# Performance work log

Hardware: AMD Instinct MI355X
Metric: run time of the kernel (lower is better)

## Reference

```python
import jax, jax.numpy as jnp
import numpy as np

HIDDEN = 2560
N_HEADS = 32
HEAD_DIM = HIDDEN // N_HEADS  # 80
ROT_DIM = int(0.4 * HEAD_DIM)  # 32, partial_rotary_factor = 0.4
MAX_POS = 2048
ROPE_THETA = 10000.0
LN_EPS = 1e-5


def _make_rope_tables(max_pos, rot_dim, theta):
    inv_freq = 1.0 / (theta ** (np.arange(0, rot_dim, 2, dtype=np.float32) / rot_dim))
    t = np.arange(max_pos, dtype=np.float32)
    freqs = np.outer(t, inv_freq)            # [max_pos, rot_dim/2]
    emb = np.concatenate([freqs, freqs], -1)  # [max_pos, rot_dim]
    return jnp.asarray(np.sin(emb)), jnp.asarray(np.cos(emb))


def setup_inputs() -> dict:
    key = jax.random.key(0)
    ks = jax.random.split(key, 16)
    B, S = 2, 2048
    std = 0.02
    sin, cos = _make_rope_tables(MAX_POS, ROT_DIM, ROPE_THETA)
    return {
        "hidden_states": jax.random.normal(ks[0], (B, S, HIDDEN), jnp.float32),
        "attention_mask": jnp.ones((B, S), jnp.int32),
        "position_ids": jnp.broadcast_to(jnp.arange(S, dtype=jnp.int32), (B, S)),
        "sin": sin, "cos": cos,
        "Wq": std * jax.random.normal(ks[1], (HIDDEN, HIDDEN), jnp.float32),
        "bq": jnp.zeros((HIDDEN,), jnp.float32),
        "Wk": std * jax.random.normal(ks[2], (HIDDEN, HIDDEN), jnp.float32),
        "bk": jnp.zeros((HIDDEN,), jnp.float32),
        "Wv": std * jax.random.normal(ks[3], (HIDDEN, HIDDEN), jnp.float32),
        "bv": jnp.zeros((HIDDEN,), jnp.float32),
        "Wo": std * jax.random.normal(ks[4], (HIDDEN, HIDDEN), jnp.float32),
        "bo": jnp.zeros((HIDDEN,), jnp.float32),
        "q_ln_scale": jnp.ones((HIDDEN,), jnp.float32),
        "q_ln_bias": jnp.zeros((HIDDEN,), jnp.float32),
        "k_ln_scale": jnp.ones((HIDDEN,), jnp.float32),
        "k_ln_bias": jnp.zeros((HIDDEN,), jnp.float32),
    }


def _layernorm(x, scale, bias):
    mu = jnp.mean(x, -1, keepdims=True)
    var = jnp.mean(jnp.square(x - mu), -1, keepdims=True)
    return (x - mu) * jax.lax.rsqrt(var + LN_EPS) * scale + bias


def _rotate_half(x):
    h = x.shape[-1] // 2
    return jnp.concatenate([-x[..., h:], x[..., :h]], -1)


def _apply_partial_rope(x, sin_p, cos_p):
    # x: [B, H, S, D]; sin_p/cos_p: [B, 1, S, ROT_DIM]
    x_rot, x_pass = x[..., :ROT_DIM], x[..., ROT_DIM:]
    x_rot = x_rot * cos_p + _rotate_half(x_rot) * sin_p
    return jnp.concatenate([x_rot, x_pass], -1)


def reference(hidden_states, attention_mask, position_ids, sin, cos,
              Wq, bq, Wk, bk, Wv, bv, Wo, bo,
              q_ln_scale, q_ln_bias, k_ln_scale, k_ln_bias):
    B, S, _ = hidden_states.shape
    q = hidden_states @ Wq + bq  # [B,S,H]
    k = hidden_states @ Wk + bk
    v = hidden_states @ Wv + bv
    # optional qk_layernorm (applied on the full projected hidden dim, as in module)
    q = _layernorm(q, q_ln_scale, q_ln_bias)
    k = _layernorm(k, k_ln_scale, k_ln_bias)
    # -> [B, nH, S, D]
    q = q.reshape(B, S, N_HEADS, HEAD_DIM).transpose(0, 2, 1, 3)
    k = k.reshape(B, S, N_HEADS, HEAD_DIM).transpose(0, 2, 1, 3)
    v = v.reshape(B, S, N_HEADS, HEAD_DIM).transpose(0, 2, 1, 3)
    sin_p = sin[position_ids][:, None, :, :]  # [B,1,S,ROT_DIM]
    cos_p = cos[position_ids][:, None, :, :]
    q = _apply_partial_rope(q, sin_p, cos_p)
    k = _apply_partial_rope(k, sin_p, cos_p)
    # causal attention with padding mask
    scores = jnp.einsum("bhqd,bhkd->bhqk", q, k) / jnp.sqrt(jnp.asarray(HEAD_DIM, q.dtype))
    causal = jnp.tril(jnp.ones((S, S), bool))[None, None]            # [1,1,S,S]
    pad = (attention_mask > 0)[:, None, None, :]                      # [B,1,1,S]
    mask = jnp.logical_and(causal, pad)
    scores = jnp.where(mask, scores, jnp.finfo(scores.dtype).min)
    attn = jax.nn.softmax(scores, axis=-1)
    out = jnp.einsum("bhqk,bhkd->bhqd", attn, v)
    out = out.transpose(0, 2, 1, 3).reshape(B, S, HIDDEN)
    return out @ Wo + bo
```

## Files before the change

kernel.cpp:

```cpp
#include <hip/hip_runtime.h>

typedef unsigned short u16;
typedef __attribute__((ext_vector_type(8))) short bf16x8;
typedef __attribute__((ext_vector_type(4))) short bf16x4;
typedef __attribute__((ext_vector_type(4))) float f32x4;

#define AS1 __attribute__((address_space(1)))
#define AS3 __attribute__((address_space(3)))

__device__ __forceinline__ float bf2f(u16 u) {
  union { unsigned int i; float f; } v; v.i = ((unsigned int)u) << 16; return v.f;
}
__device__ __forceinline__ u16 f2bf(float f) {
  union { float f; unsigned int i; } v; v.f = f;
  return (u16)((v.i + 0x7fffu + ((v.i >> 16) & 1u)) >> 16);
}

__global__ __launch_bounds__(256) void cvt_hs(const float* __restrict__ in, u16* __restrict__ out) {
  size_t i = ((size_t)blockIdx.x * 256 + threadIdx.x) * 8;
  float4 a = *(const float4*)(in + i);
  float4 b = *(const float4*)(in + i + 4);
  bf16x8 o;
  o[0] = (short)f2bf(a.x); o[1] = (short)f2bf(a.y); o[2] = (short)f2bf(a.z); o[3] = (short)f2bf(a.w);
  o[4] = (short)f2bf(b.x); o[5] = (short)f2bf(b.y); o[6] = (short)f2bf(b.z); o[7] = (short)f2bf(b.w);
  *(bf16x8*)(out + i) = o;
}

__global__ __launch_bounds__(256) void transp_k(
    const float* __restrict__ Wq, const float* __restrict__ Wk,
    const float* __restrict__ Wv, const float* __restrict__ Wo,
    u16* __restrict__ WqT, u16* __restrict__ WkT,
    u16* __restrict__ WvT, u16* __restrict__ WoT)
{
  __shared__ u16 tile[64][65];
  const float* W; u16* WT;
  switch (blockIdx.z) {
    case 0: W = Wq; WT = WqT; break;
    case 1: W = Wk; WT = WkT; break;
    case 2: W = Wv; WT = WvT; break;
    default: W = Wo; WT = WoT; break;
  }
  const int n0 = blockIdx.x * 64, k0 = blockIdx.y * 64;
  const int t = threadIdx.x;
  const int r = t >> 2, c4 = (t & 3) * 16;
  const float* src = W + (size_t)(k0 + r) * 2560 + n0 + c4;
#pragma unroll
  for (int i = 0; i < 16; i += 4) {
    float4 v = *(const float4*)(src + i);
    tile[r][c4 + i + 0] = f2bf(v.x);
    tile[r][c4 + i + 1] = f2bf(v.y);
    tile[r][c4 + i + 2] = f2bf(v.z);
    tile[r][c4 + i + 3] = f2bf(v.w);
  }
  __syncthreads();
  u16 o[16];
#pragma unroll
  for (int i = 0; i < 16; ++i) o[i] = tile[c4 + i][r];
  u16* dst = WT + (size_t)(n0 + r) * 2560 + k0 + c4;
  *(bf16x8*)dst = *(bf16x8*)&o[0];
  *(bf16x8*)(dst + 8) = *(bf16x8*)&o[8];
}

__global__ __launch_bounds__(256) void gemm_qkv(
    const u16* __restrict__ A, const u16* __restrict__ BT,
    const float* __restrict__ bq, const float* __restrict__ bk, const float* __restrict__ bv,
    u16* __restrict__ Qraw, u16* __restrict__ Kraw, u16* __restrict__ Vt)
{
  __shared__ u16 As[128 * 64];
  __shared__ u16 Bs[128 * 64];
  const int K = 2560;
  const int tid = threadIdx.x;
  const int wid = tid >> 6, lane = tid & 63;
  const int l15 = lane & 15, g = lane >> 4;
  const int m0 = blockIdx.y * 128, n0 = blockIdx.x * 128;
  const int which = blockIdx.x / 20;
  const int nn0 = n0 - which * 2560;
  const int wr = wid >> 1, wc = wid & 1;

  f32x4 acc[4][4] = {};

  const u16* aT = A + (size_t)m0 * K;
  const u16* bT = BT + (size_t)n0 * K;

  for (int k0 = 0; k0 < K; k0 += 64) {
#pragma unroll
    for (int j = 0; j < 4; ++j) {
      int off = (wid * 4 + j) * 1024 + lane * 16;
      int row = off >> 7;
      int ce  = (off & 127) >> 1;
      __builtin_amdgcn_global_load_lds(
          (const AS1 void*)(aT + (size_t)row * K + k0 + ce),
          (AS3 void*)((char*)As + (wid * 4 + j) * 1024), 16, 0, 0);
    }
#pragma unroll
    for (int j = 0; j < 4; ++j) {
      int off = (wid * 4 + j) * 1024 + lane * 16;
      int row = off >> 7;
      int ce  = (off & 127) >> 1;
      __builtin_amdgcn_global_load_lds(
          (const AS1 void*)(bT + (size_t)row * K + k0 + ce),
          (AS3 void*)((char*)Bs + (wid * 4 + j) * 1024), 16, 0, 0);
    }
    __syncthreads();
#pragma unroll
    for (int kk = 0; kk < 2; ++kk) {
      bf16x8 af[4], bfr[4];
#pragma unroll
      for (int i = 0; i < 4; ++i)
        af[i] = *(const bf16x8*)&As[(wr * 64 + i * 16 + l15) * 64 + kk * 32 + g * 8];
#pragma unroll
      for (int i = 0; i < 4; ++i)
        bfr[i] = *(const bf16x8*)&Bs[(wc * 64 + i * 16 + l15) * 64 + kk * 32 + g * 8];
#pragma unroll
      for (int i = 0; i < 4; ++i)
#pragma unroll
        for (int j = 0; j < 4; ++j)
          acc[i][j] = __builtin_amdgcn_mfma_f32_16x16x32_bf16(af[i], bfr[j], acc[i][j], 0, 0, 0);
    }
    __syncthreads();
  }

  const float* bias = (which == 0) ? bq : ((which == 1) ? bk : bv);
  float bv4[4];
#pragma unroll
  for (int j = 0; j < 4; ++j) bv4[j] = bias[nn0 + wc * 64 + j * 16 + l15];

  if (which < 2) {
    u16* out = which ? Kraw : Qraw;
#pragma unroll
    for (int i = 0; i < 4; ++i) {
      int m = m0 + wr * 64 + i * 16 + 4 * g;
#pragma unroll
      for (int j = 0; j < 4; ++j) {
        int n = nn0 + wc * 64 + j * 16 + l15;
#pragma unroll
        for (int r = 0; r < 4; ++r)
          out[(size_t)(m + r) * 2560 + n] = f2bf(acc[i][j][r] + bv4[j]);
      }
    }
  } else {
#pragma unroll
    for (int j = 0; j < 4; ++j) {
      int n = nn0 + wc * 64 + j * 16 + l15;
      int h = n / 80, d = n - h * 80;
#pragma unroll
      for (int i = 0; i < 4; ++i) {
        int m = m0 + wr * 64 + i * 16 + 4 * g;
        int b = m >> 11, s = m & 2047;
        bf16x4 pv;
#pragma unroll
        for (int r = 0; r < 4; ++r) pv[r] = (short)f2bf(acc[i][j][r] + bv4[j]);
        *(bf16x4*)&Vt[((size_t)((b * 32 + h) * 80 + d) << 11) + s] = pv;
      }
    }
  }
}

__global__ __launch_bounds__(256) void gemm_bt(
    const u16* __restrict__ A, const u16* __restrict__ BT,
    const float* __restrict__ bias, float* __restrict__ out,
    int M, int N, int K)
{
  __shared__ u16 As[128 * 64];
  __shared__ u16 Bs[128 * 64];
  const int tid = threadIdx.x;
  const int wid = tid >> 6, lane = tid & 63;
  const int l15 = lane & 15, g = lane >> 4;
  const int m0 = blockIdx.y * 128, n0 = blockIdx.x * 128;
  const int wr = wid >> 1, wc = wid & 1;

  f32x4 acc[4][4] = {};

  const u16* aT = A + (size_t)m0 * K;
  const u16* bT = BT + (size_t)n0 * K;

  for (int k0 = 0; k0 < K; k0 += 64) {
#pragma unroll
    for (int j = 0; j < 4; ++j) {
      int off = (wid * 4 + j) * 1024 + lane * 16;
      int row = off >> 7;
      int ce  = (off & 127) >> 1;
      __builtin_amdgcn_global_load_lds(
          (const AS1 void*)(aT + (size_t)row * K + k0 + ce),
          (AS3 void*)((char*)As + (wid * 4 + j) * 1024), 16, 0, 0);
    }
#pragma unroll
    for (int j = 0; j < 4; ++j) {
      int off = (wid * 4 + j) * 1024 + lane * 16;
      int row = off >> 7;
      int ce  = (off & 127) >> 1;
      __builtin_amdgcn_global_load_lds(
          (const AS1 void*)(bT + (size_t)row * K + k0 + ce),
          (AS3 void*)((char*)Bs + (wid * 4 + j) * 1024), 16, 0, 0);
    }
    __syncthreads();
#pragma unroll
    for (int kk = 0; kk < 2; ++kk) {
      bf16x8 af[4], bfr[4];
#pragma unroll
      for (int i = 0; i < 4; ++i)
        af[i] = *(const bf16x8*)&As[(wr * 64 + i * 16 + l15) * 64 + kk * 32 + g * 8];
#pragma unroll
      for (int i = 0; i < 4; ++i)
        bfr[i] = *(const bf16x8*)&Bs[(wc * 64 + i * 16 + l15) * 64 + kk * 32 + g * 8];
#pragma unroll
      for (int i = 0; i < 4; ++i)
#pragma unroll
        for (int j = 0; j < 4; ++j)
          acc[i][j] = __builtin_amdgcn_mfma_f32_16x16x32_bf16(af[i], bfr[j], acc[i][j], 0, 0, 0);
    }
    __syncthreads();
  }

  float bv4[4];
#pragma unroll
  for (int j = 0; j < 4; ++j) bv4[j] = bias[n0 + wc * 64 + j * 16 + l15];

#pragma unroll
  for (int i = 0; i < 4; ++i) {
    int m = m0 + wr * 64 + i * 16 + 4 * g;
#pragma unroll
    for (int j = 0; j < 4; ++j) {
      int n = n0 + wc * 64 + j * 16 + l15;
#pragma unroll
      for (int r = 0; r < 4; ++r)
        out[(size_t)(m + r) * N + n] = acc[i][j][r] + bv4[j];
    }
  }
}

__global__ __launch_bounds__(320) void ln_rope(
    const u16* __restrict__ Qraw, const u16* __restrict__ Kraw,
    const float* __restrict__ qsc, const float* __restrict__ qbi,
    const float* __restrict__ ksc, const float* __restrict__ kbi,
    const float* __restrict__ sinT, const float* __restrict__ cosT,
    const int* __restrict__ pos_ids,
    u16* __restrict__ Qout, u16* __restrict__ Kout)
{
  __shared__ float ybuf[2560];
  __shared__ float red[10];
  const int row = blockIdx.x;
  const int isK = blockIdx.y;
  const u16* raw   = isK ? Kraw : Qraw;
  const float* sc  = isK ? ksc : qsc;
  const float* bi  = isK ? kbi : qbi;
  u16* outp        = isK ? Kout : Qout;
  const int t = threadIdx.x;
  const int c0 = t * 8;
  bf16x8 v = *(const bf16x8*)(raw + (size_t)row * 2560 + c0);
  float x[8]; float s1 = 0.f, s2 = 0.f;
#pragma unroll
  for (int i = 0; i < 8; ++i) { x[i] = bf2f((u16)v[i]); s1 += x[i]; s2 += x[i] * x[i]; }
#pragma unroll
  for (int o = 32; o > 0; o >>= 1) { s1 += __shfl_xor(s1, o, 64); s2 += __shfl_xor(s2, o, 64); }
  const int wid = t >> 6, lane = t & 63;
  if (lane == 0) { red[wid] = s1; red[5 + wid] = s2; }
  __syncthreads();
  if (t == 0) {
    float a = 0.f, b2 = 0.f;
#pragma unroll
    for (int i = 0; i < 5; ++i) { a += red[i]; b2 += red[5 + i]; }
    red[0] = a; red[5] = b2;
  }
  __syncthreads();
  const float mean = red[0] * (1.f / 2560.f);
  const float var  = red[5] * (1.f / 2560.f) - mean * mean;
  const float rstd = rsqrtf(var + 1e-5f);
  float scv[8], biv[8];
  {
    float4 a0 = *(const float4*)(sc + c0), a1 = *(const float4*)(sc + c0 + 4);
    float4 b0 = *(const float4*)(bi + c0), b1 = *(const float4*)(bi + c0 + 4);
    scv[0]=a0.x; scv[1]=a0.y; scv[2]=a0.z; scv[3]=a0.w; scv[4]=a1.x; scv[5]=a1.y; scv[6]=a1.z; scv[7]=a1.w;
    biv[0]=b0.x; biv[1]=b0.y; biv[2]=b0.z; biv[3]=b0.w; biv[4]=b1.x; biv[5]=b1.y; biv[6]=b1.z; biv[7]=b1.w;
  }
  float y[8];
#pragma unroll
  for (int i = 0; i < 8; ++i) {
    y[i] = (x[i] - mean) * rstd * scv[i] + biv[i];
    ybuf[c0 + i] = y[i];
  }
  __syncthreads();
  const int pos = pos_ids[row];
  const int hh = c0 / 80, d0 = c0 - hh * 80;
  bf16x8 ov;
#pragma unroll
  for (int i = 0; i < 8; ++i) {
    int d = d0 + i;
    float val;
    if (d < 16) {
      val = y[i] * cosT[pos * 32 + d] - ybuf[c0 + i + 16] * sinT[pos * 32 + d];
    } else if (d < 32) {
      val = y[i] * cosT[pos * 32 + d] + ybuf[c0 + i - 16] * sinT[pos * 32 + d];
    } else {
      val = y[i];
    }
    ov[i] = (short)f2bf(val);
  }
  const int bb = row >> 11, ss = row & 2047;
  u16* obase = outp + ((size_t)(bb * 32 + hh) * 2048 + ss) * 96;
  *(bf16x8*)(obase + d0) = ov;
  if (d0 == 72) {
    bf16x8 z = {};
    *(bf16x8*)(obase + 80) = z;
    *(bf16x8*)(obase + 88) = z;
  }
}

__global__ __launch_bounds__(256, 4) void attn_k(
    const u16* __restrict__ Qr, const u16* __restrict__ Kr,
    const u16* __restrict__ Vt, const int* __restrict__ amask,
    u16* __restrict__ O)
{
  __shared__ u16 Ks[64 * 128];
  __shared__ u16 Vs[80 * 64];
  __shared__ u16 Ps[4][16 * 64];
  const int tid = threadIdx.x;
  const int wid = tid >> 6, lane = tid & 63;
  const int l15 = lane & 15, g = lane >> 4;
  const int h = blockIdx.y, b = blockIdx.z;
  const size_t bh = (size_t)b * 32 + h;
  const u16* qbase = Qr + bh * 2048 * 96;
  const u16* kbase = Kr + bh * 2048 * 96;
  const u16* vbase = Vt + bh * 80 * 2048;
  const float scl = 0.11180339887498949f;
  u16* pw = &Ps[wid][0];
  const int lsw = (l15 & 7);

  for (int ph = 0; ph < 2; ++ph) {
    const int qb = ph ? (31 - (int)blockIdx.x) : (int)blockIdx.x;
    const int qw0 = qb * 64 + wid * 16;

    bf16x8 aq[3];
    {
      const u16* qp = qbase + (size_t)(qw0 + l15) * 96;
#pragma unroll
      for (int c = 0; c < 3; ++c) aq[c] = *(const bf16x8*)(qp + c * 32 + g * 8);
    }

    f32x4 acc_o[5] = {};
    float mrow[4] = {-3e38f, -3e38f, -3e38f, -3e38f};
    float lrow[4] = {0.f, 0.f, 0.f, 0.f};
    const int ntiles = qb + 1;

    for (int t = 0; t < ntiles; ++t) {
      {
        const u16* kg = kbase + (size_t)t * 64 * 96;
#pragma unroll
        for (int j = 0; j < 4; ++j) {
          int chunk = j * 256 + tid;
          int row = chunk >> 4, scn = chunk & 15;
          int lc = scn ^ (row & 7);
          const u16* src = kg + (size_t)row * 96 + (lc < 12 ? lc * 8 : 0);
          __builtin_amdgcn_global_load_lds(
              (const AS1 void*)src,
              (AS3 void*)((char*)Ks + (j * 256 + wid * 64) * 16), 16, 0, 0);
        }
        const u16* vg = vbase + t * 64;
#pragma unroll
        for (int k2 = 0; k2 < 3; ++k2) {
          int cbase = k2 * 256 + wid * 64;
          if (cbase < 640) {
            int chunk = cbase + lane;
            int d = chunk >> 3, scn = chunk & 7;
            int lc = scn ^ (d & 7);
            const u16* src = vg + (size_t)d * 2048 + lc * 8;
            __builtin_amdgcn_global_load_lds(
                (const AS1 void*)src,
                (AS3 void*)((char*)Vs + cbase * 16), 16, 0, 0);
          }
        }
      }
      __syncthreads();

      f32x4 sacc[4] = {};
#pragma unroll
      for (int kf = 0; kf < 4; ++kf) {
#pragma unroll
        for (int c = 0; c < 3; ++c) {
          bf16x8 bk_ = *(const bf16x8*)&Ks[(kf * 16 + l15) * 128 + ((c * 4 + g) ^ lsw) * 8];
          sacc[kf] = __builtin_amdgcn_mfma_f32_16x16x32_bf16(aq[c], bk_, sacc[kf], 0, 0, 0);
        }
      }

      const int kvb0 = t * 64;
#pragma unroll
      for (int kf = 0; kf < 4; ++kf) {
        int kv = kvb0 + kf * 16 + l15;
        bool pm = amask[b * 2048 + kv] > 0;
#pragma unroll
        for (int r = 0; r < 4; ++r) {
          float sv = sacc[kf][r] * scl;
          int q = qw0 + 4 * g + r;
          if (!pm || kv > q) sv = -3e38f;
          sacc[kf][r] = sv;
        }
      }

      float p[4][4];
      float cfv[4];
#pragma unroll
      for (int r = 0; r < 4; ++r) {
        float tm = fmaxf(fmaxf(sacc[0][r], sacc[1][r]), fmaxf(sacc[2][r], sacc[3][r]));
#pragma unroll
        for (int o = 1; o < 16; o <<= 1) tm = fmaxf(tm, __shfl_xor(tm, o, 64));
        float mn = fmaxf(mrow[r], tm);
        float c = __expf(mrow[r] - mn);
        cfv[r] = c;
        mrow[r] = mn;
        float ps = 0.f;
#pragma unroll
        for (int kf = 0; kf < 4; ++kf) {
          float e = __expf(sacc[kf][r] - mn);
          p[kf][r] = e;
          ps += e;
        }
        lrow[r] = lrow[r] * c + ps;
      }
#pragma unroll
      for (int nf = 0; nf < 5; ++nf)
#pragma unroll
        for (int r = 0; r < 4; ++r) acc_o[nf][r] *= cfv[r];

#pragma unroll
      for (int kf = 0; kf < 4; ++kf)
#pragma unroll
        for (int r = 0; r < 4; ++r) {
          int prow = 4 * g + r;
          int pcol = kf * 16 + l15;
          pw[prow * 64 + ((pcol >> 3) ^ (prow & 7)) * 8 + (pcol & 7)] = f2bf(p[kf][r]);
        }

#pragma unroll
      for (int c = 0; c < 2; ++c) {
        bf16x8 ap = *(const bf16x8*)&pw[l15 * 64 + ((c * 4 + g) ^ lsw) * 8];
#pragma unroll
        for (int nf = 0; nf < 5; ++nf) {
          bf16x8 bv_ = *(const bf16x8*)&Vs[(nf * 16 + l15) * 64 + ((c * 4 + g) ^ lsw) * 8];
          acc_o[nf] = __builtin_amdgcn_mfma_f32_16x16x32_bf16(ap, bv_, acc_o[nf], 0, 0, 0);
        }
      }
      __syncthreads();
    }

#pragma unroll
    for (int r = 0; r < 4; ++r) {
      float s = lrow[r];
#pragma unroll
      for (int o = 1; o < 16; o <<= 1) s += __shfl_xor(s, o, 64);
      lrow[r] = s;
    }
#pragma unroll
    for (int nf = 0; nf < 5; ++nf) {
      int d = nf * 16 + l15;
#pragma unroll
      for (int r = 0; r < 4; ++r) {
        int q = qw0 + 4 * g + r;
        O[(size_t)(b * 2048 + q) * 2560 + h * 80 + d] = f2bf(acc_o[nf][r] / lrow[r]);
      }
    }
  }
}

extern "C" void kernel_launch(void* const* d_in, const int* in_sizes, int n_in,
                              void* d_out, int out_size, void* d_ws, size_t ws_size,
                              hipStream_t stream)
{
  const float* hs    = (const float*)d_in[0];
  const int*   amask = (const int*)d_in[1];
  const int*   pos   = (const int*)d_in[2];
  const float* sinT  = (const float*)d_in[3];
  const float* cosT  = (const float*)d_in[4];
  const float* Wq    = (const float*)d_in[5];
  const float* bq    = (const float*)d_in[6];
  const float* Wk    = (const float*)d_in[7];
  const float* bk    = (const float*)d_in[8];
  const float* Wv    = (const float*)d_in[9];
  const float* bv    = (const float*)d_in[10];
  const float* Wo    = (const float*)d_in[11];
  const float* bo    = (const float*)d_in[12];
  const float* qsc   = (const float*)d_in[13];
  const float* qbi   = (const float*)d_in[14];
  const float* ksc   = (const float*)d_in[15];
  const float* kbi   = (const float*)d_in[16];

  char* ws = (char*)d_ws;
  u16* WqT   = (u16*)(ws);
  u16* WoT   = (u16*)(ws + 39321600);
  u16* hs_bf = (u16*)(ws + 52428800);
  u16* Qraw  = (u16*)(ws + 73400320);
  u16* Kraw  = (u16*)(ws + 94371840);
  u16* Vt    = (u16*)(ws + 115343360);
  u16* Qr    = (u16*)(ws);
  u16* Kr    = (u16*)(ws + 136314880);
  u16* WkT   = WqT + 2560 * 2560;
  u16* WvT   = WkT + 2560 * 2560;
  u16* O     = Qraw;

  cvt_hs<<<dim3(5120), 256, 0, stream>>>(hs, hs_bf);
  transp_k<<<dim3(40, 40, 4), 256, 0, stream>>>(Wq, Wk, Wv, Wo, WqT, WkT, WvT, WoT);
  gemm_qkv<<<dim3(60, 32), 256, 0, stream>>>(hs_bf, WqT, bq, bk, bv, Qraw, Kraw, Vt);
  ln_rope<<<dim3(4096, 2), 320, 0, stream>>>(Qraw, Kraw, qsc, qbi, ksc, kbi, sinT, cosT, pos, Qr, Kr);
  attn_k<<<dim3(16, 32, 2), 256, 0, stream>>>(Qr, Kr, Vt, amask, O);
  gemm_bt<<<dim3(20, 32), 256, 0, stream>>>(O, WoT, bo, (float*)d_out, 4096, 2560, 2560);

  (void)in_sizes; (void)n_in; (void)out_size; (void)ws_size;
}
```

Before: 758.0 us.

## Replace both GEMMs with a double-buffered, swizzled 256x256 tile template kernel

Merges the QKV and output-projection GEMMs into one templated kernel. It uses 256x256 block tiles, 8 waves per block and a 128x64 tile per wave. Global-to-LDS loads are double-buffered with explicit vmcnt waits and barriers so the next K tile loads while MFMA runs. An XOR swizzle on the LDS column index reduces bank conflicts, and s_setprio is raised around the MFMA bursts. The larger tiles raise reuse per byte loaded, but they cut the block count: the output projection drops to 160 blocks, and the 128 KB of LDS limits each CU to one block.

```diff
diff --git a/kernel.cpp b/kernel.cpp
--- a/kernel.cpp
+++ b/kernel.cpp
@@ -61,170 +61,138 @@
   *(bf16x8*)(dst + 8) = *(bf16x8*)&o[8];
 }
 
-__global__ __launch_bounds__(256) void gemm_qkv(
+template <int MODE>
+__global__ __launch_bounds__(512, 2) void gemm256(
     const u16* __restrict__ A, const u16* __restrict__ BT,
-    const float* __restrict__ bq, const float* __restrict__ bk, const float* __restrict__ bv,
-    u16* __restrict__ Qraw, u16* __restrict__ Kraw, u16* __restrict__ Vt)
+    const float* __restrict__ b0p, const float* __restrict__ b1p, const float* __restrict__ b2p,
+    void* __restrict__ o0, void* __restrict__ o1, void* __restrict__ o2)
 {
-  __shared__ u16 As[128 * 64];
-  __shared__ u16 Bs[128 * 64];
-  const int K = 2560;
+  __shared__ u16 As[2][256 * 64];
+  __shared__ u16 Bs[2][256 * 64];
+  const int K = 2560, NT = 40;
   const int tid = threadIdx.x;
   const int wid = tid >> 6, lane = tid & 63;
   const int l15 = lane & 15, g = lane >> 4;
-  const int m0 = blockIdx.y * 128, n0 = blockIdx.x * 128;
-  const int which = blockIdx.x / 20;
-  const int nn0 = n0 - which * 2560;
-  const int wr = wid >> 1, wc = wid & 1;
-
-  f32x4 acc[4][4] = {};
-
-  const u16* aT = A + (size_t)m0 * K;
-  const u16* bT = BT + (size_t)n0 * K;
-
-  for (int k0 = 0; k0 < K; k0 += 64) {
-#pragma unroll
-    for (int j = 0; j < 4; ++j) {
-      int off = (wid * 4 + j) * 1024 + lane * 16;
-      int row = off >> 7;
-      int ce  = (off & 127) >> 1;
-      __builtin_amdgcn_global_load_lds(
-          (const AS1 void*)(aT + (size_t)row * K + k0 + ce),
-          (AS3 void*)((char*)As + (wid * 4 + j) * 1024), 16, 0, 0);
-    }
-#pragma unroll
-    for (int j = 0; j < 4; ++j) {
-      int off = (wid * 4 + j) * 1024 + lane * 16;
-      int row = off >> 7;
-      int ce  = (off & 127) >> 1;
-      __builtin_amdgcn_global_load_lds(
-          (const AS1 void*)(bT + (size_t)row * K + k0 + ce),
-          (AS3 void*)((char*)Bs + (wid * 4 + j) * 1024), 16, 0, 0);
-    }
-    __syncthreads();
+  const int wm = wid >> 2, wn = wid & 3;
+  const int m0 = blockIdx.y * 256, n0 = blockIdx.x * 256;
+
+  const int srow = tid >> 3;
+  const int slc  = (tid & 7) ^ (srow & 7);
+  const u16* aT = A + (size_t)(m0 + srow) * K + slc * 8;
+  const u16* bT = BT + (size_t)(n0 + srow) * K + slc * 8;
+
+#define STAGE(pb, kt)                                                              \
+  {                                                                                \
+    const u16* a_ = aT + (size_t)(kt) * 64;                                        \
+    const u16* b_ = bT + (size_t)(kt) * 64;                                        \
+    char* la = (char*)&As[pb][0] + wid * 1024 + lane * 16;                         \
+    char* lb = (char*)&Bs[pb][0] + wid * 1024 + lane * 16;                         \
+    _Pragma("unroll")                                                              \
+    for (int i_ = 0; i_ < 4; ++i_) {                                               \
+      __builtin_amdgcn_global_load_lds((const AS1 void*)(a_ + (size_t)i_ * 64 * K),\
+                                       (AS3 void*)(la + i_ * 8192), 16, 0, 0);     \
+      __builtin_amdgcn_global_load_lds((const AS1 void*)(b_ + (size_t)i_ * 64 * K),\
+                                       (AS3 void*)(lb + i_ * 8192), 16, 0, 0);     \
+    }                                                                              \
+  }
+
+  f32x4 acc[8][4] = {};
+
+  STAGE(0, 0);
+  STAGE(1, 1);
+  asm volatile("s_waitcnt vmcnt(8)" ::: "memory");
+  __builtin_amdgcn_s_barrier();
+  __builtin_amdgcn_sched_barrier(0);
+
+  for (int t = 0; t < NT; ++t) {
+    const int p = t & 1;
+    const u16* as = &As[p][0];
+    const u16* bs = &Bs[p][0];
 #pragma unroll
     for (int kk = 0; kk < 2; ++kk) {
-      bf16x8 af[4], bfr[4];
-#pragma unroll
-      for (int i = 0; i < 4; ++i)
-        af[i] = *(const bf16x8*)&As[(wr * 64 + i * 16 + l15) * 64 + kk * 32 + g * 8];
-#pragma unroll
-      for (int i = 0; i < 4; ++i)
-        bfr[i] = *(const bf16x8*)&Bs[(wc * 64 + i * 16 + l15) * 64 + kk * 32 + g * 8];
-#pragma unroll
-      for (int i = 0; i < 4; ++i)
-#pragma unroll
-        for (int j = 0; j < 4; ++j)
-          acc[i][j] = __builtin_amdgcn_mfma_f32_16x16x32_bf16(af[i], bfr[j], acc[i][j], 0, 0, 0);
-    }
-    __syncthreads();
-  }
-
-  const float* bias = (which == 0) ? bq : ((which == 1) ? bk : bv);
-  float bv4[4];
-#pragma unroll
-  for (int j = 0; j < 4; ++j) bv4[j] = bias[nn0 + wc * 64 + j * 16 + l15];
-
-  if (which < 2) {
-    u16* out = which ? Kraw : Qraw;
-#pragma unroll
-    for (int i = 0; i < 4; ++i) {
-      int m = m0 + wr * 64 + i * 16 + 4 * g;
-#pragma unroll
-      for (int j = 0; j < 4; ++j) {
-        int n = nn0 + wc * 64 + j * 16 + l15;
+      bf16x8 af[8], bfv[4];
+      const int cj = ((kk * 4 + g) ^ (l15 & 7)) * 8;
+#pragma unroll
+      for (int m = 0; m < 8; ++m)
+        af[m] = *(const bf16x8*)&as[(wm * 128 + m * 16 + l15) * 64 + cj];
+#pragma unroll
+      for (int n = 0; n < 4; ++n)
+        bfv[n] = *(const bf16x8*)&bs[(wn * 64 + n * 16 + l15) * 64 + cj];
+      __builtin_amdgcn_s_setprio(1);
+#pragma unroll
+      for (int m = 0; m < 8; ++m)
+#pragma unroll
+        for (int n = 0; n < 4; ++n)
+          acc[m][n] = __builtin_amdgcn_mfma_f32_16x16x32_bf16(af[m], bfv[n], acc[m][n], 0, 0, 0);
+      __builtin_amdgcn_s_setprio(0);
+    }
+    __builtin_amdgcn_s_barrier();
+    __builtin_amdgcn_sched_barrier(0);
+    if (t + 2 < NT) {
+      STAGE(p, t + 2);
+      asm volatile("s_waitcnt vmcnt(8)" ::: "memory");
+      __builtin_amdgcn_s_barrier();
+      __builtin_amdgcn_sched_barrier(0);
+    } else if (t + 1 < NT) {
+      asm volatile("s_waitcnt vmcnt(0)" ::: "memory");
+      __builtin_amdgcn_s_barrier();
+      __builtin_amdgcn_sched_barrier(0);
+    }
+  }
+#undef STAGE
+
+  if (MODE == 0) {
+    const int which = n0 / 2560;
+    const int nn0 = n0 - which * 2560;
+    const float* bias = (which == 0) ? b0p : ((which == 1) ? b1p : b2p);
+    float bvv[4];
+#pragma unroll
+    for (int n = 0; n < 4; ++n) bvv[n] = bias[nn0 + wn * 64 + n * 16 + l15];
+    if (which < 2) {
+      u16* out = which ? (u16*)o1 : (u16*)o0;
+#pragma unroll
+      for (int m = 0; m < 8; ++m) {
+        int mm = m0 + wm * 128 + m * 16 + 4 * g;
+#pragma unroll
+        for (int n = 0; n < 4; ++n) {
+          int nn = nn0 + wn * 64 + n * 16 + l15;
+#pragma unroll
+          for (int r = 0; r < 4; ++r)
+            out[(size_t)(mm + r) * 2560 + nn] = f2bf(acc[m][n][r] + bvv[n]);
+        }
+      }
+    } else {
+      u16* Vt = (u16*)o2;
+#pragma unroll
+      for (int n = 0; n < 4; ++n) {
+        int nn = nn0 + wn * 64 + n * 16 + l15;
+        int h = nn / 80, d = nn - h * 80;
+#pragma unroll
+        for (int m = 0; m < 8; ++m) {
+          int mm = m0 + wm * 128 + m * 16 + 4 * g;
+          int b = mm >> 11, s = mm & 2047;
+          bf16x4 pv;
+#pragma unroll
+          for (int r = 0; r < 4; ++r) pv[r] = (short)f2bf(acc[m][n][r] + bvv[n]);
+          *(bf16x4*)&Vt[((size_t)((b * 32 + h) * 80 + d) << 11) + s] = pv;
+        }
+      }
+    }
+  } else {
+    float* out = (float*)o0;
+    float bvv[4];
+#pragma unroll
+    for (int n = 0; n < 4; ++n) bvv[n] = b0p[n0 + wn * 64 + n * 16 + l15];
+#pragma unroll
+    for (int m = 0; m < 8; ++m) {
+      int mm = m0 + wm * 128 + m * 16 + 4 * g;
+#pragma unroll
+      for (int n = 0; n < 4; ++n) {
+        int nn = n0 + wn * 64 + n * 16 + l15;
 #pragma unroll
         for (int r = 0; r < 4; ++r)
-          out[(size_t)(m + r) * 2560 + n] = f2bf(acc[i][j][r] + bv4[j]);
-      }
-    }
-  } else {
-#pragma unroll
-    for (int j = 0; j < 4; ++j) {
-      int n = nn0 + wc * 64 + j * 16 + l15;
-      int h = n / 80, d = n - h * 80;
-#pragma unroll
-      for (int i = 0; i < 4; ++i) {
-        int m = m0 + wr * 64 + i * 16 + 4 * g;
-        int b = m >> 11, s = m & 2047;
-        bf16x4 pv;
-#pragma unroll
-        for (int r = 0; r < 4; ++r) pv[r] = (short)f2bf(acc[i][j][r] + bv4[j]);
-        *(bf16x4*)&Vt[((size_t)((b * 32 + h) * 80 + d) << 11) + s] = pv;
-      }
-    }
-  }
-}
-
-__global__ __launch_bounds__(256) void gemm_bt(
-    const u16* __restrict__ A, const u16* __restrict__ BT,
-    const float* __restrict__ bias, float* __restrict__ out,
-    int M, int N, int K)
-{
-  __shared__ u16 As[128 * 64];
-  __shared__ u16 Bs[128 * 64];
-  const int tid = threadIdx.x;
-  const int wid = tid >> 6, lane = tid & 63;
-  const int l15 = lane & 15, g = lane >> 4;
-  const int m0 = blockIdx.y * 128, n0 = blockIdx.x * 128;
-  const int wr = wid >> 1, wc = wid & 1;
-
-  f32x4 acc[4][4] = {};
-
-  const u16* aT = A + (size_t)m0 * K;
-  const u16* bT = BT + (size_t)n0 * K;
-
-  for (int k0 = 0; k0 < K; k0 += 64) {
-#pragma unroll
-    for (int j = 0; j < 4; ++j) {
-      int off = (wid * 4 + j) * 1024 + lane * 16;
-      int row = off >> 7;
-      int ce  = (off & 127) >> 1;
-      __builtin_amdgcn_global_load_lds(
-          (const AS1 void*)(aT + (size_t)row * K + k0 + ce),
-          (AS3 void*)((char*)As + (wid * 4 + j) * 1024), 16, 0, 0);
-    }
-#pragma unroll
-    for (int j = 0; j < 4; ++j) {
-      int off = (wid * 4 + j) * 1024 + lane * 16;
-      int row = off >> 7;
-      int ce  = (off & 127) >> 1;
-      __builtin_amdgcn_global_load_lds(
-          (const AS1 void*)(bT + (size_t)row * K + k0 + ce),
-          (AS3 void*)((char*)Bs + (wid * 4 + j) * 1024), 16, 0, 0);
-    }
-    __syncthreads();
-#pragma unroll
-    for (int kk = 0; kk < 2; ++kk) {
-      bf16x8 af[4], bfr[4];
-#pragma unroll
-      for (int i = 0; i < 4; ++i)
-        af[i] = *(const bf16x8*)&As[(wr * 64 + i * 16 + l15) * 64 + kk * 32 + g * 8];
-#pragma unroll
-      for (int i = 0; i < 4; ++i)
-        bfr[i] = *(const bf16x8*)&Bs[(wc * 64 + i * 16 + l15) * 64 + kk * 32 + g * 8];
-#pragma unroll
-      for (int i = 0; i < 4; ++i)
-#pragma unroll
-        for (int j = 0; j < 4; ++j)
-          acc[i][j] = __builtin_amdgcn_mfma_f32_16x16x32_bf16(af[i], bfr[j], acc[i][j], 0, 0, 0);
-    }
-    __syncthreads();
-  }
-
-  float bv4[4];
-#pragma unroll
-  for (int j = 0; j < 4; ++j) bv4[j] = bias[n0 + wc * 64 + j * 16 + l15];
-
-#pragma unroll
-  for (int i = 0; i < 4; ++i) {
-    int m = m0 + wr * 64 + i * 16 + 4 * g;
-#pragma unroll
-    for (int j = 0; j < 4; ++j) {
-      int n = n0 + wc * 64 + j * 16 + l15;
-#pragma unroll
-      for (int r = 0; r < 4; ++r)
-        out[(size_t)(m + r) * N + n] = acc[i][j][r] + bv4[j];
+          out[(size_t)(mm + r) * 2560 + nn] = acc[m][n][r] + bvv[n];
+      }
     }
   }
 }
@@ -498,10 +466,10 @@
 
   cvt_hs<<<dim3(5120), 256, 0, stream>>>(hs, hs_bf);
   transp_k<<<dim3(40, 40, 4), 256, 0, stream>>>(Wq, Wk, Wv, Wo, WqT, WkT, WvT, WoT);
-  gemm_qkv<<<dim3(60, 32), 256, 0, stream>>>(hs_bf, WqT, bq, bk, bv, Qraw, Kraw, Vt);
+  gemm256<0><<<dim3(30, 16), 512, 0, stream>>>(hs_bf, WqT, bq, bk, bv, Qraw, Kraw, Vt);
   ln_rope<<<dim3(4096, 2), 320, 0, stream>>>(Qraw, Kraw, qsc, qbi, ksc, kbi, sinT, cosT, pos, Qr, Kr);
   attn_k<<<dim3(16, 32, 2), 256, 0, stream>>>(Qr, Kr, Vt, amask, O);
-  gemm_bt<<<dim3(20, 32), 256, 0, stream>>>(O, WoT, bo, (float*)d_out, 4096, 2560, 2560);
+  gemm256<1><<<dim3(10, 16), 512, 0, stream>>>(O, WoT, bo, nullptr, nullptr, d_out, nullptr, nullptr);
 
   (void)in_sizes; (void)n_in; (void)out_size; (void)ws_size;
 }
```

Result: faster. 659.6 us (-13.0%).
